# Kernel tuning notes

Measured on AMD Instinct MI355X. Metric: run time of the kernel, lower is better.

## Reference

```python
import jax, jax.numpy as jnp
import numpy as np

N = 524288   # total spokes
D = 128      # dim_hidden
B = 128      # graphs in batch
H = 64       # hubs per graph (static, num_hubs_type='S')
K = 4        # hubs_per_spoke


def setup_inputs() -> dict:
    key = jax.random.key(0)
    ks = jax.random.split(key, 5)
    x = jax.random.normal(ks[0], (N, D), jnp.float32)
    spoke_init_hub_idx = jax.random.randint(ks[1], (N,), 0, H)
    batch_idx = jnp.sort(jax.random.randint(ks[2], (N,), 0, B))
    s1 = 1.0 / np.sqrt(D)
    s2 = 1.0 / np.sqrt(2 * D)
    W1 = jax.random.uniform(ks[3], (D, 2 * D), jnp.float32, -s1, s1)
    b1 = jnp.zeros((2 * D,), jnp.float32)
    W2 = jax.random.uniform(ks[4], (2 * D, D), jnp.float32, -s2, s2)
    b2 = jnp.zeros((D,), jnp.float32)
    return {"x": x, "spoke_init_hub_idx": spoke_init_hub_idx, "batch_idx": batch_idx,
            "W1": W1, "b1": b1, "W2": W2, "b2": b2}


def reference(x, spoke_init_hub_idx, batch_idx, W1, b1, W2, b2):
    # FeedForward on spokes: Linear -> GELU(exact, torch default) -> Linear
    h = jax.nn.gelu(x @ W1 + b1, approximate=False) @ W2 + b2  # [N, D]

    # batched hub index: local hub idx offset by graph (uniform H hubs/graph)
    gidx = batch_idx * H + spoke_init_hub_idx  # [N]

    # scatter_mean of spoke features into hubs (empty hubs -> 0, as torch scatter_mean)
    sums = jax.ops.segment_sum(h, gidx, num_segments=B * H)                    # [B*H, D]
    cnt = jax.ops.segment_sum(jnp.ones((N,), h.dtype), gidx, num_segments=B * H)
    hub_features = sums / jnp.maximum(cnt, 1.0)[:, None]                       # [B*H, D]

    # assign each spoke to the K hubs closest to its initial hub (within its graph)
    hf = hub_features.reshape(B, H, D)
    d2 = jnp.sum((hf[:, :, None, :] - hf[:, None, :, :]) ** 2, axis=-1)        # [B, H, H]
    _, knn = jax.lax.top_k(-d2, K)                                             # [B, H, K] local hub ids
    hubs_idx = knn[batch_idx, spoke_init_hub_idx] + batch_idx[:, None] * H     # [N, K] global hub ids
    spokes_idx = jnp.repeat(jnp.arange(N), K)
    spokes_hubs_edge_index = jnp.stack([spokes_idx, hubs_idx.reshape(-1)], axis=0)  # [2, N*K]

    return hub_features, spokes_hubs_edge_index
```

## Files before the change

### kernel.cpp

```cpp
#include <hip/hip_runtime.h>
#include <hip/hip_bf16.h>

#define N_SPOKES 524288
#define DIM      128
#define DIM2     256
#define NB       128
#define NH       64
#define BH       8192

#define OUT_HF   0
#define OUT_E0   1048576
#define OUT_E1   3145728

typedef __attribute__((ext_vector_type(8))) short  short8;
typedef __attribute__((ext_vector_type(4))) float  float4v;
typedef __attribute__((ext_vector_type(4))) unsigned short ushort4v;

__device__ inline unsigned short f2bf(float f) {
    __hip_bfloat16 h = __float2bfloat16(f);
    return *reinterpret_cast<unsigned short*>(&h);
}

__device__ inline unsigned int pkbf(float a, float b) {
    __hip_bfloat162 h = __float22bfloat162_rn(make_float2(a, b));
    union { __hip_bfloat162 h; unsigned int u; } cv;
    cv.h = h;
    return cv.u;
}

__device__ inline float gelu_f(float v) {
    float s = v * (1.0f + 0.044715f * v * v);
    float e = __builtin_exp2f(-2.302118131f * s);
    return v * __builtin_amdgcn_rcpf(1.0f + e);
}

__global__ void setup_kernel(const int* __restrict__ batchidx, const int* __restrict__ hubidx,
                             const float* __restrict__ W1,
                             unsigned short* __restrict__ w1t,
                             int* __restrict__ goff, int* __restrict__ cnt) {
    int b = blockIdx.x, tid = threadIdx.x;
    if (b < 2048) {
        int i = b * 256 + tid;
        if (i < N_SPOKES) {
            int bi = batchidx[i];
            int bp = (i == 0) ? -1 : batchidx[i - 1];
            for (int g = bp + 1; g <= bi; ++g) goff[g] = i;
            if (i == N_SPOKES - 1)
                for (int g = bi + 1; g <= NB; ++g) goff[g] = N_SPOKES;
            atomicAdd(&cnt[bi * NH + hubidx[i]], 1);
        }
    } else {
        int idx = (b - 2048) * 256 + tid;
        if (idx < DIM * DIM2) {
            int n = idx >> 7, k = idx & 127;
            w1t[idx] = f2bf(W1[k * DIM2 + n]);
        }
    }
}

__launch_bounds__(512, 4)
__global__ void ffn_fused(const float* __restrict__ x,
                          const int* __restrict__ hubidx,
                          const int* __restrict__ goff,
                          const unsigned short* __restrict__ w1t,
                          const float* __restrict__ b1,
                          float* __restrict__ outbuf,
                          int atomic_mode) {
    __shared__ unsigned short sA[128 * 136];
    __shared__ unsigned short sU[256 * 40];
    __shared__ unsigned short sOne[64 * 136];

    const int tid  = threadIdx.x;
    const int lane = tid & 63;
    const int w    = tid >> 6;
    const int c_lo = lane & 15;
    const int c_hi = lane >> 4;
    const int wcb  = w * 32;
    const int g      = blockIdx.x >> 2;
    const int cchunk = blockIdx.x & 3;

    const int s = goff[g], e = goff[g + 1];
    const int len = e - s;
    const int cs  = (len + 3) >> 2;
    const int ms  = s + cchunk * cs;
    int me = ms + cs; if (me > e) me = e;
    const int n  = me - ms;
    const int nt = (n > 0) ? ((n + 127) >> 7) : 0;

    short8 bfr[2][4];
    #pragma unroll
    for (int n4 = 0; n4 < 2; ++n4)
        #pragma unroll
        for (int k = 0; k < 4; ++k) {
            int col = wcb + n4 * 16 + c_lo;
            bfr[n4][k] = *(const short8*)(w1t + col * DIM + k * 32 + c_hi * 8);
        }
    float bcol[2];
    #pragma unroll
    for (int n4 = 0; n4 < 2; ++n4) bcol[n4] = b1[wcb + n4 * 16 + c_lo];

    float4v hacc[4][2];
    #pragma unroll
    for (int mt = 0; mt < 4; ++mt)
        #pragma unroll
        for (int n4 = 0; n4 < 2; ++n4) hacc[mt][n4] = (float4v){0.f, 0.f, 0.f, 0.f};

    for (int i = tid; i < 2048; i += 512)
        *(unsigned long long*)&sOne[(i >> 5) * 136 + (i & 31) * 4] = 0ULL;

    const float4v* x4 = (const float4v*)x;

    int hub_nxt = -1;
    if (nt > 0 && tid < 128) hub_nxt = (tid < n) ? hubidx[ms + tid] : -1;
    __syncthreads();

    for (int t = 0; t < nt; ++t) {
        const int hub_cur = hub_nxt;

        {
            float4v ld[8];
            #pragma unroll
            for (int it = 0; it < 8; ++it) {
                int f = it * 512 + tid;
                int r = t * 128 + (f >> 5);
                int rr = r < n ? r : n - 1;
                ld[it] = x4[(size_t)(ms + rr) * 32 + (f & 31)];
            }
            if (tid < 128 && hub_cur >= 0)
                sOne[hub_cur * 136 + tid] = (unsigned short)0x3F80;
            #pragma unroll
            for (int it = 0; it < 8; ++it) {
                int f = it * 512 + tid;
                int row = f >> 5, c4 = f & 31;
                float4v v = ld[it];
                unsigned int lo = pkbf(v.x, v.y);
                unsigned int hi = pkbf(v.z, v.w);
                *(uint2*)&sA[row * 136 + c4 * 4] = make_uint2(lo, hi);
            }
        }
        __syncthreads();

        if (t + 1 < nt && tid < 128) {
            int r = (t + 1) * 128 + tid;
            hub_nxt = (r < n) ? hubidx[ms + r] : -1;
        }

        #pragma unroll
        for (int ks = 0; ks < 4; ++ks) {
            float4v acc[2][2];
            #pragma unroll
            for (int m2 = 0; m2 < 2; ++m2)
                #pragma unroll
                for (int n4 = 0; n4 < 2; ++n4) acc[m2][n4] = (float4v){0.f, 0.f, 0.f, 0.f};

            #pragma unroll
            for (int k = 0; k < 4; ++k)
                #pragma unroll
                for (int m2 = 0; m2 < 2; ++m2) {
                    short8 a = *(const short8*)&sA[(ks * 32 + m2 * 16 + c_lo) * 136 + k * 32 + c_hi * 8];
                    acc[m2][0] = __builtin_amdgcn_mfma_f32_16x16x32_bf16(a, bfr[0][k], acc[m2][0], 0, 0, 0);
                    acc[m2][1] = __builtin_amdgcn_mfma_f32_16x16x32_bf16(a, bfr[1][k], acc[m2][1], 0, 0, 0);
                }

            #pragma unroll
            for (int m2 = 0; m2 < 2; ++m2) {
                int rbase = m2 * 16 + c_hi * 4;
                #pragma unroll
                for (int n4 = 0; n4 < 2; ++n4) {
                    int col = wcb + n4 * 16 + c_lo;
                    float4v a4 = acc[m2][n4];
                    unsigned int lo = pkbf(gelu_f(a4.x + bcol[n4]), gelu_f(a4.y + bcol[n4]));
                    unsigned int hi = pkbf(gelu_f(a4.z + bcol[n4]), gelu_f(a4.w + bcol[n4]));
                    *(uint2*)&sU[col * 40 + rbase] = make_uint2(lo, hi);
                }
            }

            short8 aS[4];
            #pragma unroll
            for (int mt = 0; mt < 4; ++mt)
                aS[mt] = *(const short8*)&sOne[(mt * 16 + c_lo) * 136 + ks * 32 + c_hi * 8];
            short8 bU[2];
            #pragma unroll
            for (int n4 = 0; n4 < 2; ++n4)
                bU[n4] = *(const short8*)&sU[(wcb + n4 * 16 + c_lo) * 40 + c_hi * 8];
            #pragma unroll
            for (int mt = 0; mt < 4; ++mt)
                #pragma unroll
                for (int n4 = 0; n4 < 2; ++n4)
                    hacc[mt][n4] = __builtin_amdgcn_mfma_f32_16x16x32_bf16(aS[mt], bU[n4], hacc[mt][n4], 0, 0, 0);
        }
        __syncthreads();
        if (tid < 128 && hub_cur >= 0)
            sOne[hub_cur * 136 + tid] = 0;
    }

    #pragma unroll
    for (int mt = 0; mt < 4; ++mt)
        #pragma unroll
        for (int n4 = 0; n4 < 2; ++n4) {
            float4v v = hacc[mt][n4];
            int col = wcb + n4 * 16 + c_lo;
            #pragma unroll
            for (int reg = 0; reg < 4; ++reg) {
                int hub = mt * 16 + c_hi * 4 + reg;
                size_t o = ((size_t)g * NH + hub) * DIM2 + col;
                if (atomic_mode) atomicAdd(&outbuf[o], v[reg]);
                else outbuf[(size_t)cchunk * BH * DIM2 + o] = v[reg];
            }
        }
}

__global__ void hubfeat_kernel(const float* __restrict__ part, int nchunk,
                               const int* __restrict__ cnt,
                               const float* __restrict__ W2, const float* __restrict__ b2,
                               float* __restrict__ out) {
    __shared__ float sSum[16 * 256];
    int tid = threadIdx.x;
    int d   = tid & 127;
    int hh  = tid >> 7;

    for (int i = tid; i < 16 * 256; i += 256) {
        size_t o = (size_t)(blockIdx.x * 16) * DIM2 + i;
        float v = 0.f;
        for (int c = 0; c < nchunk; ++c) v += part[(size_t)c * BH * DIM2 + o];
        sSum[i] = v;
    }
    __syncthreads();

    int h0 = hh * 8;
    float acc[8] = {0.f, 0.f, 0.f, 0.f, 0.f, 0.f, 0.f, 0.f};
    for (int k4 = 0; k4 < 64; ++k4) {
        float w0 = W2[(k4 * 4 + 0) * DIM + d];
        float w1 = W2[(k4 * 4 + 1) * DIM + d];
        float w2 = W2[(k4 * 4 + 2) * DIM + d];
        float w3 = W2[(k4 * 4 + 3) * DIM + d];
        #pragma unroll
        for (int j = 0; j < 8; ++j) {
            float4v sv = *(const float4v*)&sSum[(h0 + j) * 256 + k4 * 4];
            acc[j] += sv.x * w0 + sv.y * w1 + sv.z * w2 + sv.w * w3;
        }
    }
    float b2d = b2[d];
    #pragma unroll
    for (int j = 0; j < 8; ++j) {
        int h = blockIdx.x * 16 + h0 + j;
        float c = (float)cnt[h];
        out[OUT_HF + h * DIM + d] = (acc[j] + c * b2d) / fmaxf(c, 1.0f);
    }
}

__global__ void knn_edges(const float* __restrict__ hf, const int* __restrict__ goff,
                          const int* __restrict__ hubidx, float* __restrict__ out) {
    __shared__ float s[64 * 129];
    __shared__ float d2[64 * 64];
    __shared__ int sK[64 * 4];
    int g = blockIdx.x, tid = threadIdx.x;

    for (int i = tid; i < 64 * 128; i += 256) {
        int r = i >> 7, c = i & 127;
        s[r * 129 + c] = hf[OUT_HF + (g * 64 + r) * DIM + c];
    }
    __syncthreads();

    for (int p = tid; p < 4096; p += 256) {
        int i = p >> 6, j = p & 63;
        float a = 0.f;
        for (int k = 0; k < 128; ++k) {
            float dd = s[i * 129 + k] - s[j * 129 + k];
            a += dd * dd;
        }
        d2[p] = a;
    }
    __syncthreads();

    if (tid < 64) {
        float bv0 = 1e30f, bv1 = 1e30f, bv2 = 1e30f, bv3 = 1e30f;
        int   bi0 = 0,     bi1 = 0,     bi2 = 0,     bi3 = 0;
        for (int j = 0; j < 64; ++j) {
            float v = d2[tid * 64 + j];
            if (v < bv0)      { bv3=bv2; bi3=bi2; bv2=bv1; bi2=bi1; bv1=bv0; bi1=bi0; bv0=v; bi0=j; }
            else if (v < bv1) { bv3=bv2; bi3=bi2; bv2=bv1; bi2=bi1; bv1=v;   bi1=j; }
            else if (v < bv2) { bv3=bv2; bi3=bi2; bv2=v;   bi2=j; }
            else if (v < bv3) { bv3=v;   bi3=j; }
        }
        sK[tid * 4 + 0] = bi0; sK[tid * 4 + 1] = bi1;
        sK[tid * 4 + 2] = bi2; sK[tid * 4 + 3] = bi3;
    }
    __syncthreads();

    int sgs = goff[g], sge = goff[g + 1];
    float gbase = (float)(g * NH);
    for (int i = sgs + tid; i < sge; i += 256) {
        int h = hubidx[i];
        int4 kn = *(const int4*)&sK[h * 4];
        float fi = (float)i;
        float4v o0 = { fi, fi, fi, fi };
        ((float4v*)(out + OUT_E0))[i] = o0;
        float4v o1 = { kn.x + gbase, kn.y + gbase, kn.z + gbase, kn.w + gbase };
        ((float4v*)(out + OUT_E1))[i] = o1;
    }
}

extern "C" void kernel_launch(void* const* d_in, const int* in_sizes, int n_in,
                              void* d_out, int out_size, void* d_ws, size_t ws_size,
                              hipStream_t stream) {
    const float* x        = (const float*)d_in[0];
    const int*   hubidx   = (const int*)d_in[1];
    const int*   batchidx = (const int*)d_in[2];
    const float* W1       = (const float*)d_in[3];
    const float* b1       = (const float*)d_in[4];
    const float* W2       = (const float*)d_in[5];
    const float* b2       = (const float*)d_in[6];
    float* out = (float*)d_out;
    char*  ws  = (char*)d_ws;

    const size_t need_partial = 33654784;
    int atomic_mode = (ws_size < need_partial) ? 1 : 0;

    float*          part;
    int*            cnt;
    unsigned short* w1t;
    int*            goff;
    if (!atomic_mode) {
        part = (float*)ws;
        cnt  = (int*)(ws + 33554432);
        w1t  = (unsigned short*)(ws + 33587200);
        goff = (int*)(ws + 33652736);
    } else {
        part = (float*)ws;
        cnt  = (int*)(ws + 8388608);
        w1t  = (unsigned short*)(ws + 8421376);
        goff = (int*)(ws + 8486912);
    }

    (void)hipMemsetAsync(cnt, 0, 32768, stream);
    if (atomic_mode) (void)hipMemsetAsync(part, 0, 8388608, stream);

    setup_kernel<<<2176, 256, 0, stream>>>(batchidx, hubidx, W1, w1t, goff, cnt);
    ffn_fused   <<<512,  512, 0, stream>>>(x, hubidx, goff, w1t, b1, part, atomic_mode);
    hubfeat_kernel<<<512, 256, 0, stream>>>(part, atomic_mode ? 1 : 4, cnt, W2, b2, out);
    knn_edges   <<<NB,   256, 0, stream>>>(out, goff, hubidx, out);
}
```

Baseline: 516.8 us.

## Double-buffer spoke tiles in fused FFN and halve chunks per graph

The fused FFN kernel now keeps two LDS buffers for the bf16 input tile and the one-hot hub matrix. It prefetches the next tile's x rows into registers while the current tile's MFMAs run, and drops the trailing barrier and one-hot clear by clearing the stale buffer lazily. Each graph is split into 2 chunks instead of 4, which halves the grid to 256 blocks, shrinks the partial-sum workspace and gives the reduction kernel fewer partials to read. In exchange, LDS use and register pressure rise (launch bounds lowered to 2 blocks per SM), and there are fewer blocks to cover the GPU.

```diff
diff --git a/kernel.cpp b/kernel.cpp
--- a/kernel.cpp
+++ b/kernel.cpp
@@ -58,7 +58,7 @@
     }
 }
 
-__launch_bounds__(512, 4)
+__launch_bounds__(512, 2)
 __global__ void ffn_fused(const float* __restrict__ x,
                           const int* __restrict__ hubidx,
                           const int* __restrict__ goff,
@@ -66,9 +66,9 @@
                           const float* __restrict__ b1,
                           float* __restrict__ outbuf,
                           int atomic_mode) {
-    __shared__ unsigned short sA[128 * 136];
+    __shared__ unsigned short sA[2][128 * 136];
     __shared__ unsigned short sU[256 * 40];
-    __shared__ unsigned short sOne[64 * 136];
+    __shared__ unsigned short sOne[2][64 * 136];
 
     const int tid  = threadIdx.x;
     const int lane = tid & 63;
@@ -76,12 +76,12 @@
     const int c_lo = lane & 15;
     const int c_hi = lane >> 4;
     const int wcb  = w * 32;
-    const int g      = blockIdx.x >> 2;
-    const int cchunk = blockIdx.x & 3;
+    const int g      = blockIdx.x >> 1;
+    const int cchunk = blockIdx.x & 1;
 
     const int s = goff[g], e = goff[g + 1];
     const int len = e - s;
-    const int cs  = (len + 3) >> 2;
+    const int cs  = (len + 1) >> 1;
     const int ms  = s + cchunk * cs;
     int me = ms + cs; if (me > e) me = e;
     const int n  = me - ms;
@@ -105,44 +105,62 @@
         #pragma unroll
         for (int n4 = 0; n4 < 2; ++n4) hacc[mt][n4] = (float4v){0.f, 0.f, 0.f, 0.f};
 
-    for (int i = tid; i < 2048; i += 512)
-        *(unsigned long long*)&sOne[(i >> 5) * 136 + (i & 31) * 4] = 0ULL;
+    for (int i = tid; i < 4096; i += 512) {
+        int b = i >> 11, r = (i >> 5) & 63, c = i & 31;
+        *(unsigned long long*)&sOne[b][r * 136 + c * 4] = 0ULL;
+    }
 
     const float4v* x4 = (const float4v*)x;
 
+    float4v ld[8];
     int hub_nxt = -1;
-    if (nt > 0 && tid < 128) hub_nxt = (tid < n) ? hubidx[ms + tid] : -1;
+    int hubA = -1, hubB = -1;
+    if (nt > 0) {
+        #pragma unroll
+        for (int it = 0; it < 8; ++it) {
+            int f = it * 512 + tid;
+            int r = f >> 5;
+            int rr = r < n ? r : n - 1;
+            ld[it] = x4[(size_t)(ms + rr) * 32 + (f & 31)];
+        }
+        if (tid < 128) hub_nxt = (tid < n) ? hubidx[ms + tid] : -1;
+    }
     __syncthreads();
 
     for (int t = 0; t < nt; ++t) {
+        const int p = t & 1;
         const int hub_cur = hub_nxt;
-
-        {
-            float4v ld[8];
+        const int hclear  = p ? hubB : hubA;
+
+        if (tid < 128) {
+            if (hclear >= 0)  sOne[p][hclear * 136 + tid] = 0;
+            if (hub_cur >= 0) sOne[p][hub_cur * 136 + tid] = (unsigned short)0x3F80;
+        }
+        if (p) hubB = hub_cur; else hubA = hub_cur;
+
+        #pragma unroll
+        for (int it = 0; it < 8; ++it) {
+            int f = it * 512 + tid;
+            int row = f >> 5, c4 = f & 31;
+            float4v v = ld[it];
+            unsigned int lo = pkbf(v.x, v.y);
+            unsigned int hi = pkbf(v.z, v.w);
+            *(uint2*)&sA[p][row * 136 + c4 * 4] = make_uint2(lo, hi);
+        }
+        __syncthreads();
+
+        if (t + 1 < nt) {
             #pragma unroll
             for (int it = 0; it < 8; ++it) {
                 int f = it * 512 + tid;
-                int r = t * 128 + (f >> 5);
+                int r = (t + 1) * 128 + (f >> 5);
                 int rr = r < n ? r : n - 1;
                 ld[it] = x4[(size_t)(ms + rr) * 32 + (f & 31)];
             }
-            if (tid < 128 && hub_cur >= 0)
-                sOne[hub_cur * 136 + tid] = (unsigned short)0x3F80;
-            #pragma unroll
-            for (int it = 0; it < 8; ++it) {
-                int f = it * 512 + tid;
-                int row = f >> 5, c4 = f & 31;
-                float4v v = ld[it];
-                unsigned int lo = pkbf(v.x, v.y);
-                unsigned int hi = pkbf(v.z, v.w);
-                *(uint2*)&sA[row * 136 + c4 * 4] = make_uint2(lo, hi);
+            if (tid < 128) {
+                int r = (t + 1) * 128 + tid;
+                hub_nxt = (r < n) ? hubidx[ms + r] : -1;
             }
-        }
-        __syncthreads();
-
-        if (t + 1 < nt && tid < 128) {
-            int r = (t + 1) * 128 + tid;
-            hub_nxt = (r < n) ? hubidx[ms + r] : -1;
         }
 
         #pragma unroll
@@ -157,7 +175,7 @@
             for (int k = 0; k < 4; ++k)
                 #pragma unroll
                 for (int m2 = 0; m2 < 2; ++m2) {
-                    short8 a = *(const short8*)&sA[(ks * 32 + m2 * 16 + c_lo) * 136 + k * 32 + c_hi * 8];
+                    short8 a = *(const short8*)&sA[p][(ks * 32 + m2 * 16 + c_lo) * 136 + k * 32 + c_hi * 8];
                     acc[m2][0] = __builtin_amdgcn_mfma_f32_16x16x32_bf16(a, bfr[0][k], acc[m2][0], 0, 0, 0);
                     acc[m2][1] = __builtin_amdgcn_mfma_f32_16x16x32_bf16(a, bfr[1][k], acc[m2][1], 0, 0, 0);
                 }
@@ -178,7 +196,7 @@
             short8 aS[4];
             #pragma unroll
             for (int mt = 0; mt < 4; ++mt)
-                aS[mt] = *(const short8*)&sOne[(mt * 16 + c_lo) * 136 + ks * 32 + c_hi * 8];
+                aS[mt] = *(const short8*)&sOne[p][(mt * 16 + c_lo) * 136 + ks * 32 + c_hi * 8];
             short8 bU[2];
             #pragma unroll
             for (int n4 = 0; n4 < 2; ++n4)
@@ -189,9 +207,6 @@
                 for (int n4 = 0; n4 < 2; ++n4)
                     hacc[mt][n4] = __builtin_amdgcn_mfma_f32_16x16x32_bf16(aS[mt], bU[n4], hacc[mt][n4], 0, 0, 0);
         }
-        __syncthreads();
-        if (tid < 128 && hub_cur >= 0)
-            sOne[hub_cur * 136 + tid] = 0;
     }
 
     #pragma unroll
@@ -314,7 +329,7 @@
     float* out = (float*)d_out;
     char*  ws  = (char*)d_ws;
 
-    const size_t need_partial = 33654784;
+    const size_t need_partial = 16879616;
     int atomic_mode = (ws_size < need_partial) ? 1 : 0;
 
     float*          part;
@@ -323,9 +338,9 @@
     int*            goff;
     if (!atomic_mode) {
         part = (float*)ws;
-        cnt  = (int*)(ws + 33554432);
-        w1t  = (unsigned short*)(ws + 33587200);
-        goff = (int*)(ws + 33652736);
+        cnt  = (int*)(ws + 16777216);
+        w1t  = (unsigned short*)(ws + 16809984);
+        goff = (int*)(ws + 16875520);
     } else {
         part = (float*)ws;
         cnt  = (int*)(ws + 8388608);
@@ -337,7 +352,7 @@
     if (atomic_mode) (void)hipMemsetAsync(part, 0, 8388608, stream);
 
     setup_kernel<<<2176, 256, 0, stream>>>(batchidx, hubidx, W1, w1t, goff, cnt);
-    ffn_fused   <<<512,  512, 0, stream>>>(x, hubidx, goff, w1t, b1, part, atomic_mode);
-    hubfeat_kernel<<<512, 256, 0, stream>>>(part, atomic_mode ? 1 : 4, cnt, W2, b2, out);
+    ffn_fused   <<<256,  512, 0, stream>>>(x, hubidx, goff, w1t, b1, part, atomic_mode);
+    hubfeat_kernel<<<512, 256, 0, stream>>>(part, atomic_mode ? 1 : 2, cnt, W2, b2, out);
     knn_edges   <<<NB,   256, 0, stream>>>(out, goff, hubidx, out);
 }
```

Result: faster. 492.8 us (-4.7%).
